# Optimization experiments

Measured on AMD Instinct MI355X. Metric: run time of the kernel, lower is better.

Reference implementation:

```python
import jax, jax.numpy as jnp
import numpy as np

N = 100000      # nodes
E = 3200000     # edges (avg degree 32)
IN = 256        # in_channels
OUT = 8         # out_channels
H1, C1 = 4, 4   # conv1: heads=4, out_channels=4 (concat -> 16)


def setup_inputs() -> dict:
    key = jax.random.key(0)
    ks = jax.random.split(key, 10)
    x = jax.random.normal(ks[0], (N, IN), jnp.float32)
    edge_index = jax.random.randint(ks[1], (2, E), 0, N, dtype=jnp.int64)

    def glorot(k, shape):
        fan_in = shape[0]
        return jax.random.normal(k, shape, jnp.float32) / np.float32(np.sqrt(fan_in))

    W1l = glorot(ks[2], (IN, H1 * C1))
    W1r = glorot(ks[3], (IN, H1 * C1))
    a1 = jax.random.normal(ks[4], (H1, C1), jnp.float32) / np.float32(np.sqrt(C1))
    b1 = jnp.zeros((H1 * C1,), jnp.float32)
    W2l = glorot(ks[5], (H1 * C1, OUT))
    W2r = glorot(ks[6], (H1 * C1, OUT))
    a2 = jax.random.normal(ks[7], (1, OUT), jnp.float32) / np.float32(np.sqrt(OUT))
    b2 = jnp.zeros((OUT,), jnp.float32)
    return {"x": x, "edge_index": edge_index, "W1l": W1l, "W1r": W1r, "a1": a1,
            "b1": b1, "W2l": W2l, "W2r": W2r, "a2": a2, "b2": b2}


def gatv2_conv(x, edge_index, Wl, Wr, att, bias, heads, ch, concat):
    # GATv2: e_ij = a^T LeakyReLU(Wl x_j + Wr x_i), softmax over incoming edges of i
    n = x.shape[0]
    src, dst = edge_index[0], edge_index[1]          # message flows src -> dst
    xl = (x @ Wl).reshape(n, heads, ch)              # [N,H,C] (source transform)
    xr = (x @ Wr).reshape(n, heads, ch)              # [N,H,C] (target transform)
    e = jax.nn.leaky_relu(xl[src] + xr[dst], 0.2)    # [E,H,C]
    logits = jnp.einsum('ehc,hc->eh', e, att)        # [E,H]
    # segment softmax over dst (stable: subtract per-target max)
    m = jax.ops.segment_max(logits, dst, num_segments=n)          # [N,H]
    ex = jnp.exp(logits - m[dst])                                  # [E,H]
    denom = jax.ops.segment_sum(ex, dst, num_segments=n)          # [N,H]
    alpha = ex / (denom[dst] + 1e-16)                              # [E,H]
    out = jax.ops.segment_sum(alpha[:, :, None] * xl[src], dst, num_segments=n)  # [N,H,C]
    out = out.reshape(n, heads * ch) if concat else out.mean(axis=1)
    return out + bias


def reference(x, edge_index, W1l, W1r, a1, b1, W2l, W2r, a2, b2):
    # eval mode: feature/attention dropout (p=0.6) are identity
    h = jax.nn.elu(gatv2_conv(x, edge_index, W1l, W1r, a1, b1, H1, C1, True))
    h = gatv2_conv(h, edge_index, W2l, W2r, a2, b2, 1, OUT, False)
    return jax.nn.sigmoid(h)
```

## Files before the change

### kernel.cpp

```cpp
#include <hip/hip_runtime.h>
#include <math.h>

#define NN 100000
#define NE 3200000
#define BW 512
#define BSH 9
#define NB 196
#define EPB_A 8192
#define NBLK_A ((NE + EPB_A - 1) / EPB_A)

__device__ __forceinline__ float lrelu(float v) { return v >= 0.f ? v : 0.2f * v; }


__global__ __launch_bounds__(256) void k_bhist(const int* __restrict__ dst,
                                               unsigned* __restrict__ btot) {
  __shared__ unsigned lh[NB];
  int tid = threadIdx.x;
  if (tid < NB) lh[tid] = 0;
  __syncthreads();
  int base = blockIdx.x * EPB_A;
  int end = min(base + EPB_A, NE);
  for (int e = base + tid * 4; e < end; e += 1024) {
    int4 d4 = *(const int4*)(dst + e);
    atomicAdd(&lh[((unsigned)d4.x) >> BSH], 1u);
    atomicAdd(&lh[((unsigned)d4.y) >> BSH], 1u);
    atomicAdd(&lh[((unsigned)d4.z) >> BSH], 1u);
    atomicAdd(&lh[((unsigned)d4.w) >> BSH], 1u);
  }
  __syncthreads();
  if (tid < NB && lh[tid]) atomicAdd(&btot[tid], lh[tid]);
}

__global__ __launch_bounds__(256) void k_bscan(const unsigned* __restrict__ btot,
    unsigned* __restrict__ bstart, unsigned* __restrict__ bcur) {
  __shared__ unsigned sm[256];
  int tid = threadIdx.x;
  unsigned v = (tid < NB) ? btot[tid] : 0;
  sm[tid] = v;
  __syncthreads();
  for (int off = 1; off < 256; off <<= 1) {
    unsigned u = (tid >= off) ? sm[tid - off] : 0;
    __syncthreads();
    sm[tid] += u;
    __syncthreads();
  }
  unsigned exc = sm[tid] - v;
  if (tid < NB) { bstart[tid] = exc; bcur[tid] = exc; }
  if (tid == NB - 1) bstart[NB] = sm[tid];
}

__global__ __launch_bounds__(256) void k_bin(const int* __restrict__ src,
    const int* __restrict__ dst, unsigned* __restrict__ bcur,
    unsigned* __restrict__ abuf) {
  __shared__ unsigned lh[NB], gb[NB], lcur[NB];
  int tid = threadIdx.x;
  if (tid < NB) lh[tid] = 0;
  __syncthreads();
  int base = blockIdx.x * EPB_A;
  int end = min(base + EPB_A, NE);
  for (int e = base + tid * 4; e < end; e += 1024) {
    int4 d4 = *(const int4*)(dst + e);
    atomicAdd(&lh[((unsigned)d4.x) >> BSH], 1u);
    atomicAdd(&lh[((unsigned)d4.y) >> BSH], 1u);
    atomicAdd(&lh[((unsigned)d4.z) >> BSH], 1u);
    atomicAdd(&lh[((unsigned)d4.w) >> BSH], 1u);
  }
  __syncthreads();
  if (tid < NB) {
    unsigned c = lh[tid];
    gb[tid] = c ? atomicAdd(&bcur[tid], c) : 0u;
    lcur[tid] = 0;
  }
  __syncthreads();
  for (int e = base + tid * 4; e < end; e += 1024) {
    int4 d4 = *(const int4*)(dst + e);
    int4 s4 = *(const int4*)(src + e);
    #pragma unroll
    for (int k = 0; k < 4; ++k) {
      unsigned d = (unsigned)(&d4.x)[k];
      unsigned s = (unsigned)(&s4.x)[k];
      unsigned b = d >> BSH;
      unsigned p = gb[b] + atomicAdd(&lcur[b], 1u);
      abuf[p] = ((d & (BW - 1)) << 17) | s;
    }
  }
}

__global__ __launch_bounds__(256) void k_bsort(const unsigned* __restrict__ bstart,
    const unsigned* __restrict__ abuf, int* __restrict__ rowstart,
    int* __restrict__ cnt, int* __restrict__ ssrc) {
  __shared__ unsigned lh[BW];
  __shared__ unsigned lcur[BW];
  __shared__ unsigned sm[256];
  int b = blockIdx.x, tid = threadIdx.x;
  unsigned s0 = bstart[b], s1 = bstart[b + 1];
  lh[tid] = 0; lh[tid + 256] = 0;
  __syncthreads();
  for (unsigned i = s0 + tid; i < s1; i += 256)
    atomicAdd(&lh[abuf[i] >> 17], 1u);
  __syncthreads();
  unsigned a0 = lh[2 * tid], a1 = lh[2 * tid + 1];
  sm[tid] = a0 + a1;
  __syncthreads();
  for (int off = 1; off < 256; off <<= 1) {
    unsigned u = (tid >= off) ? sm[tid - off] : 0;
    __syncthreads();
    sm[tid] += u;
    __syncthreads();
  }
  unsigned exc = sm[tid] - (a0 + a1);
  int node = b * BW + 2 * tid;
  if (node < NN)     { rowstart[node]     = s0 + exc;      cnt[node]     = a0; }
  if (node + 1 < NN) { rowstart[node + 1] = s0 + exc + a0; cnt[node + 1] = a1; }
  lcur[2 * tid] = exc;
  lcur[2 * tid + 1] = exc + a0;
  __syncthreads();
  for (unsigned i = s0 + tid; i < s1; i += 256) {
    unsigned v = abuf[i];
    unsigned p = s0 + atomicAdd(&lcur[v >> 17], 1u);
    ssrc[p] = (int)(v & 0x1FFFFu);
  }
}


__global__ __launch_bounds__(256) void k1_lin1(const float* __restrict__ x,
    const float* __restrict__ W1l, const float* __restrict__ W1r,
    float* __restrict__ xl1, float* __restrict__ xr1) {
  __shared__ float lw[256][32];
  int tid = threadIdx.x;
  for (int i = tid; i < 256 * 16; i += 256) {
    int k = i >> 4, c = i & 15;
    lw[k][c]      = W1l[i];
    lw[k][16 + c] = W1r[i];
  }
  __syncthreads();
  int row = blockIdx.x * 8 + (tid >> 5);
  if (row >= NN) return;
  int col = tid & 31;
  const float4* xrow = (const float4*)(x + (size_t)row * 256);
  float acc = 0.f;
  #pragma unroll 8
  for (int k4 = 0; k4 < 64; ++k4) {
    float4 xv = xrow[k4];
    int k = k4 << 2;
    acc = fmaf(xv.x, lw[k][col], acc);
    acc = fmaf(xv.y, lw[k + 1][col], acc);
    acc = fmaf(xv.z, lw[k + 2][col], acc);
    acc = fmaf(xv.w, lw[k + 3][col], acc);
  }
  if (col < 16) xl1[row * 16 + col] = acc;
  else          xr1[row * 16 + (col - 16)] = acc;
}


__global__ __launch_bounds__(256) void k_l1(const float* __restrict__ xl1,
    const float* __restrict__ xr1, const float* __restrict__ a1,
    const float* __restrict__ b1, const float* __restrict__ W2l,
    const float* __restrict__ W2r, const int* __restrict__ rowstart,
    const int* __restrict__ cnt, const int* __restrict__ ssrc,
    float* __restrict__ xl2, float* __restrict__ xr2) {
  __shared__ float w2[16][16];
  int tid = threadIdx.x;
  if (tid < 128) {
    int k = tid >> 3, c = tid & 7;
    w2[k][c]     = W2l[tid];
    w2[k][8 + c] = W2r[tid];
  }
  __syncthreads();
  int i = blockIdx.x * 256 + tid;
  if (i >= NN) return;

  float av[16];
  #pragma unroll
  for (int c = 0; c < 16; ++c) av[c] = a1[c];
  float xr[16];
  {
    const float4* xrp = (const float4*)(xr1 + (size_t)i * 16);
    #pragma unroll
    for (int q = 0; q < 4; ++q) *(float4*)&xr[q * 4] = xrp[q];
  }

  int rs = rowstart[i], deg = cnt[i];
  float m[4], den[4], acc[16];
  #pragma unroll
  for (int h = 0; h < 4; ++h) { m[h] = -INFINITY; den[h] = 0.f; }
  #pragma unroll
  for (int c = 0; c < 16; ++c) acc[c] = 0.f;

  float xn[16];
  if (deg > 0) {
    int s0 = ssrc[rs];
    const float4* xp = (const float4*)(xl1 + (size_t)s0 * 16);
    #pragma unroll
    for (int q = 0; q < 4; ++q) *(float4*)&xn[q * 4] = xp[q];
  }
  for (int j = 0; j < deg; ++j) {
    float xl[16];
    #pragma unroll
    for (int c = 0; c < 16; ++c) xl[c] = xn[c];
    if (j + 1 < deg) {
      int s = ssrc[rs + j + 1];
      const float4* xp = (const float4*)(xl1 + (size_t)s * 16);
      #pragma unroll
      for (int q = 0; q < 4; ++q) *(float4*)&xn[q * 4] = xp[q];
    }
    #pragma unroll
    for (int h = 0; h < 4; ++h) {
      float lg = lrelu(xl[h*4+0] + xr[h*4+0]) * av[h*4+0]
               + lrelu(xl[h*4+1] + xr[h*4+1]) * av[h*4+1]
               + lrelu(xl[h*4+2] + xr[h*4+2]) * av[h*4+2]
               + lrelu(xl[h*4+3] + xr[h*4+3]) * av[h*4+3];
      float nm = fmaxf(m[h], lg);
      float r = __expf(m[h] - nm);
      float p = __expf(lg - nm);
      m[h] = nm;
      den[h] = den[h] * r + p;
      #pragma unroll
      for (int c = 0; c < 4; ++c)
        acc[h*4+c] = acc[h*4+c] * r + p * xl[h*4+c];
    }
  }

  float hh[16];
  #pragma unroll
  for (int c = 0; c < 16; ++c) {
    float v = acc[c] / (den[c >> 2] + 1e-16f) + b1[c];
    hh[c] = v > 0.f ? v : expm1f(v);
  }
  float ol[8], orr[8];
  #pragma unroll
  for (int j = 0; j < 8; ++j) { ol[j] = 0.f; orr[j] = 0.f; }
  #pragma unroll
  for (int k = 0; k < 16; ++k) {
    float hv = hh[k];
    #pragma unroll
    for (int j = 0; j < 8; ++j) {
      ol[j]  = fmaf(hv, w2[k][j], ol[j]);
      orr[j] = fmaf(hv, w2[k][8 + j], orr[j]);
    }
  }
  *(float4*)(xl2 + (size_t)i * 8)     = make_float4(ol[0], ol[1], ol[2], ol[3]);
  *(float4*)(xl2 + (size_t)i * 8 + 4) = make_float4(ol[4], ol[5], ol[6], ol[7]);
  *(float4*)(xr2 + (size_t)i * 8)     = make_float4(orr[0], orr[1], orr[2], orr[3]);
  *(float4*)(xr2 + (size_t)i * 8 + 4) = make_float4(orr[4], orr[5], orr[6], orr[7]);
}


__global__ __launch_bounds__(256) void k_l2(const float* __restrict__ xl2,
    const float* __restrict__ xr2, const float* __restrict__ a2,
    const float* __restrict__ b2, const int* __restrict__ rowstart,
    const int* __restrict__ cnt, const int* __restrict__ ssrc,
    float* __restrict__ out) {
  int i = blockIdx.x * 256 + threadIdx.x;
  if (i >= NN) return;

  float av[8];
  #pragma unroll
  for (int c = 0; c < 8; ++c) av[c] = a2[c];
  float xr[8];
  {
    const float4* xrp = (const float4*)(xr2 + (size_t)i * 8);
    *(float4*)&xr[0] = xrp[0];
    *(float4*)&xr[4] = xrp[1];
  }

  int rs = rowstart[i], deg = cnt[i];
  float m = -INFINITY, den = 0.f, acc[8];
  #pragma unroll
  for (int c = 0; c < 8; ++c) acc[c] = 0.f;

  float xn[8];
  if (deg > 0) {
    int s0 = ssrc[rs];
    const float4* xp = (const float4*)(xl2 + (size_t)s0 * 8);
    *(float4*)&xn[0] = xp[0];
    *(float4*)&xn[4] = xp[1];
  }
  for (int j = 0; j < deg; ++j) {
    float xl[8];
    #pragma unroll
    for (int c = 0; c < 8; ++c) xl[c] = xn[c];
    if (j + 1 < deg) {
      int s = ssrc[rs + j + 1];
      const float4* xp = (const float4*)(xl2 + (size_t)s * 8);
      *(float4*)&xn[0] = xp[0];
      *(float4*)&xn[4] = xp[1];
    }
    float lg = 0.f;
    #pragma unroll
    for (int c = 0; c < 8; ++c) lg += lrelu(xl[c] + xr[c]) * av[c];
    float nm = fmaxf(m, lg);
    float r = __expf(m - nm);
    float p = __expf(lg - nm);
    m = nm;
    den = den * r + p;
    #pragma unroll
    for (int c = 0; c < 8; ++c) acc[c] = acc[c] * r + p * xl[c];
  }

  float o[8];
  #pragma unroll
  for (int c = 0; c < 8; ++c) {
    float v = acc[c] / (den + 1e-16f) + b2[c];
    o[c] = 1.f / (1.f + __expf(-v));
  }
  *(float4*)(out + (size_t)i * 8)     = make_float4(o[0], o[1], o[2], o[3]);
  *(float4*)(out + (size_t)i * 8 + 4) = make_float4(o[4], o[5], o[6], o[7]);
}


extern "C" void kernel_launch(void* const* d_in, const int* in_sizes, int n_in,
                              void* d_out, int out_size, void* d_ws, size_t ws_size,
                              hipStream_t stream) {
  const float* x   = (const float*)d_in[0];
  const int*   ei  = (const int*)d_in[1];
  const float* W1l = (const float*)d_in[2];
  const float* W1r = (const float*)d_in[3];
  const float* a1  = (const float*)d_in[4];
  const float* b1  = (const float*)d_in[5];
  const float* W2l = (const float*)d_in[6];
  const float* W2r = (const float*)d_in[7];
  const float* a2  = (const float*)d_in[8];
  const float* b2  = (const float*)d_in[9];
  const int* src = ei;
  const int* dst = ei + NE;

  char* ws = (char*)d_ws;
  size_t off = 0;
  auto alloc = [&](size_t bytes) { void* p = (void*)(ws + off); off += (bytes + 255) & ~(size_t)255; return p; };
  unsigned* btot   = (unsigned*)alloc((size_t)NB * 4);
  unsigned* bstart = (unsigned*)alloc((size_t)(NB + 1) * 4);
  unsigned* bcur   = (unsigned*)alloc((size_t)NB * 4);
  int*      rowstart = (int*)alloc((size_t)NN * 4);
  int*      cnt      = (int*)alloc((size_t)NN * 4);
  int*      ssrc     = (int*)alloc((size_t)NE * 4);
  char*     bigbase  = (char*)alloc((size_t)NN * 16 * 4 * 2);
  unsigned* abuf = (unsigned*)bigbase;
  float*    xl1  = (float*)bigbase;
  float*    xr1  = (float*)(bigbase + (size_t)NN * 16 * 4);
  float*    xl2  = (float*)alloc((size_t)NN * 8 * 4);
  float*    xr2  = (float*)alloc((size_t)NN * 8 * 4);

  hipMemsetAsync(btot, 0, (size_t)NB * 4, stream);

  k_bhist<<<NBLK_A, 256, 0, stream>>>(dst, btot);
  k_bscan<<<1, 256, 0, stream>>>(btot, bstart, bcur);
  k_bin  <<<NBLK_A, 256, 0, stream>>>(src, dst, bcur, abuf);
  k_bsort<<<NB, 256, 0, stream>>>(bstart, abuf, rowstart, cnt, ssrc);

  k1_lin1<<<(NN + 7) / 8, 256, 0, stream>>>(x, W1l, W1r, xl1, xr1);

  int gn = (NN + 255) / 256;
  k_l1<<<gn, 256, 0, stream>>>(xl1, xr1, a1, b1, W2l, W2r, rowstart, cnt, ssrc, xl2, xr2);
  k_l2<<<gn, 256, 0, stream>>>(xl2, xr2, a2, b2, rowstart, cnt, ssrc, (float*)d_out);
}
```

Baseline: 504.6 us.

## Use one wavefront per node for attention aggregation and thread-per-row linear

Both attention kernels now assign a 64-lane wavefront to each destination node. Neighbors are spread across lanes, and the kernel uses a chunked online softmax with shuffle max and sum reductions. Before, one thread walked the whole degree serially, with divergent, uncoalesced loads. The first linear layer switches from one thread per output column to one thread per row computing all 32 outputs, which reuses LDS weights via float4 broadcasts. The risks are wasted lanes for low-degree nodes (average degree 32 against wave width 64), more reduction overhead, and strided per-thread x row reads in lin1.

```diff
diff --git a/kernel.cpp b/kernel.cpp
--- a/kernel.cpp
+++ b/kernel.cpp
@@ -134,22 +134,45 @@
     lw[k][16 + c] = W1r[i];
   }
   __syncthreads();
-  int row = blockIdx.x * 8 + (tid >> 5);
+  int row = blockIdx.x * 256 + tid;
   if (row >= NN) return;
-  int col = tid & 31;
-  const float4* xrow = (const float4*)(x + (size_t)row * 256);
-  float acc = 0.f;
-  #pragma unroll 8
-  for (int k4 = 0; k4 < 64; ++k4) {
-    float4 xv = xrow[k4];
-    int k = k4 << 2;
-    acc = fmaf(xv.x, lw[k][col], acc);
-    acc = fmaf(xv.y, lw[k + 1][col], acc);
-    acc = fmaf(xv.z, lw[k + 2][col], acc);
-    acc = fmaf(xv.w, lw[k + 3][col], acc);
-  }
-  if (col < 16) xl1[row * 16 + col] = acc;
-  else          xr1[row * 16 + (col - 16)] = acc;
+  const float4* xr4 = (const float4*)(x + (size_t)row * 256);
+
+  float acc[32];
+  #pragma unroll
+  for (int c = 0; c < 32; ++c) acc[c] = 0.f;
+
+  float4 va = xr4[0], vb = xr4[1];
+  for (int k4 = 0; k4 < 64; k4 += 2) {
+    float4 vc = xr4[(k4 + 2) & 63];
+    float4 vd = xr4[(k4 + 3) & 63];
+    #pragma unroll
+    for (int half = 0; half < 2; ++half) {
+      float4 v = half ? vb : va;
+      int kb = (k4 + half) * 4;
+      #pragma unroll
+      for (int kk = 0; kk < 4; ++kk) {
+        float xk = (&v.x)[kk];
+        const float4* wrow = (const float4*)&lw[kb + kk][0];
+        #pragma unroll
+        for (int q = 0; q < 8; ++q) {
+          float4 w = wrow[q];
+          acc[q * 4 + 0] = fmaf(xk, w.x, acc[q * 4 + 0]);
+          acc[q * 4 + 1] = fmaf(xk, w.y, acc[q * 4 + 1]);
+          acc[q * 4 + 2] = fmaf(xk, w.z, acc[q * 4 + 2]);
+          acc[q * 4 + 3] = fmaf(xk, w.w, acc[q * 4 + 3]);
+        }
+      }
+    }
+    va = vc; vb = vd;
+  }
+  float4* ol = (float4*)(xl1 + (size_t)row * 16);
+  float4* orr = (float4*)(xr1 + (size_t)row * 16);
+  #pragma unroll
+  for (int q = 0; q < 4; ++q) {
+    ol[q]  = make_float4(acc[q*4+0], acc[q*4+1], acc[q*4+2], acc[q*4+3]);
+    orr[q] = make_float4(acc[16+q*4+0], acc[16+q*4+1], acc[16+q*4+2], acc[16+q*4+3]);
+  }
 }
 
 
@@ -167,82 +190,75 @@
     w2[k][8 + c] = W2r[tid];
   }
   __syncthreads();
-  int i = blockIdx.x * 256 + tid;
+  int i = (blockIdx.x * 256 + tid) >> 6;
   if (i >= NN) return;
-
-  float av[16];
-  #pragma unroll
-  for (int c = 0; c < 16; ++c) av[c] = a1[c];
-  float xr[16];
-  {
-    const float4* xrp = (const float4*)(xr1 + (size_t)i * 16);
-    #pragma unroll
-    for (int q = 0; q < 4; ++q) *(float4*)&xr[q * 4] = xrp[q];
-  }
-
+  int lane = tid & 63;
+  int j = lane >> 2, h = lane & 3;
+
+  float4 xr = *(const float4*)(xr1 + (size_t)i * 16 + h * 4);
+  float4 av = *(const float4*)(a1 + h * 4);
   int rs = rowstart[i], deg = cnt[i];
-  float m[4], den[4], acc[16];
-  #pragma unroll
-  for (int h = 0; h < 4; ++h) { m[h] = -INFINITY; den[h] = 0.f; }
-  #pragma unroll
-  for (int c = 0; c < 16; ++c) acc[c] = 0.f;
-
-  float xn[16];
-  if (deg > 0) {
-    int s0 = ssrc[rs];
-    const float4* xp = (const float4*)(xl1 + (size_t)s0 * 16);
-    #pragma unroll
-    for (int q = 0; q < 4; ++q) *(float4*)&xn[q * 4] = xp[q];
-  }
-  for (int j = 0; j < deg; ++j) {
-    float xl[16];
-    #pragma unroll
-    for (int c = 0; c < 16; ++c) xl[c] = xn[c];
-    if (j + 1 < deg) {
-      int s = ssrc[rs + j + 1];
-      const float4* xp = (const float4*)(xl1 + (size_t)s * 16);
-      #pragma unroll
-      for (int q = 0; q < 4; ++q) *(float4*)&xn[q * 4] = xp[q];
-    }
-    #pragma unroll
-    for (int h = 0; h < 4; ++h) {
-      float lg = lrelu(xl[h*4+0] + xr[h*4+0]) * av[h*4+0]
-               + lrelu(xl[h*4+1] + xr[h*4+1]) * av[h*4+1]
-               + lrelu(xl[h*4+2] + xr[h*4+2]) * av[h*4+2]
-               + lrelu(xl[h*4+3] + xr[h*4+3]) * av[h*4+3];
-      float nm = fmaxf(m[h], lg);
-      float r = __expf(m[h] - nm);
-      float p = __expf(lg - nm);
-      m[h] = nm;
-      den[h] = den[h] * r + p;
-      #pragma unroll
-      for (int c = 0; c < 4; ++c)
-        acc[h*4+c] = acc[h*4+c] * r + p * xl[h*4+c];
-    }
-  }
+
+  float m = -INFINITY, den = 0.f;
+  float4 acc = make_float4(0.f, 0.f, 0.f, 0.f);
+
+  for (int base = 0; base < deg; base += 16) {
+    int jj = base + j;
+    bool valid = jj < deg;
+    int s = valid ? ssrc[rs + jj] : 0;
+    float4 xl = make_float4(0.f, 0.f, 0.f, 0.f);
+    if (valid) xl = *(const float4*)(xl1 + (size_t)s * 16 + h * 4);
+    float lg = valid ? (lrelu(xl.x + xr.x) * av.x + lrelu(xl.y + xr.y) * av.y +
+                        lrelu(xl.z + xr.z) * av.z + lrelu(xl.w + xr.w) * av.w)
+                     : -INFINITY;
+    float mp = lg;
+    mp = fmaxf(mp, __shfl_xor(mp, 4));
+    mp = fmaxf(mp, __shfl_xor(mp, 8));
+    mp = fmaxf(mp, __shfl_xor(mp, 16));
+    mp = fmaxf(mp, __shfl_xor(mp, 32));
+    float nm = fmaxf(m, mp);
+    float r = __expf(m - nm);
+    float p = __expf(lg - nm);
+    m = nm;
+    den = den * r + p;
+    acc.x = acc.x * r + p * xl.x;
+    acc.y = acc.y * r + p * xl.y;
+    acc.z = acc.z * r + p * xl.z;
+    acc.w = acc.w * r + p * xl.w;
+  }
+  #pragma unroll
+  for (int st = 4; st <= 32; st <<= 1) {
+    den   += __shfl_xor(den, st);
+    acc.x += __shfl_xor(acc.x, st);
+    acc.y += __shfl_xor(acc.y, st);
+    acc.z += __shfl_xor(acc.z, st);
+    acc.w += __shfl_xor(acc.w, st);
+  }
+  float4 bv = *(const float4*)(b1 + h * 4);
+  float inv = 1.f / (den + 1e-16f);
+  float q0 = acc.x * inv + bv.x;
+  float q1 = acc.y * inv + bv.y;
+  float q2 = acc.z * inv + bv.z;
+  float q3 = acc.w * inv + bv.w;
+  q0 = q0 > 0.f ? q0 : expm1f(q0);
+  q1 = q1 > 0.f ? q1 : expm1f(q1);
+  q2 = q2 > 0.f ? q2 : expm1f(q2);
+  q3 = q3 > 0.f ? q3 : expm1f(q3);
 
   float hh[16];
   #pragma unroll
-  for (int c = 0; c < 16; ++c) {
-    float v = acc[c] / (den[c >> 2] + 1e-16f) + b1[c];
-    hh[c] = v > 0.f ? v : expm1f(v);
-  }
-  float ol[8], orr[8];
-  #pragma unroll
-  for (int j = 0; j < 8; ++j) { ol[j] = 0.f; orr[j] = 0.f; }
-  #pragma unroll
-  for (int k = 0; k < 16; ++k) {
-    float hv = hh[k];
-    #pragma unroll
-    for (int j = 0; j < 8; ++j) {
-      ol[j]  = fmaf(hv, w2[k][j], ol[j]);
-      orr[j] = fmaf(hv, w2[k][8 + j], orr[j]);
-    }
-  }
-  *(float4*)(xl2 + (size_t)i * 8)     = make_float4(ol[0], ol[1], ol[2], ol[3]);
-  *(float4*)(xl2 + (size_t)i * 8 + 4) = make_float4(ol[4], ol[5], ol[6], ol[7]);
-  *(float4*)(xr2 + (size_t)i * 8)     = make_float4(orr[0], orr[1], orr[2], orr[3]);
-  *(float4*)(xr2 + (size_t)i * 8 + 4) = make_float4(orr[4], orr[5], orr[6], orr[7]);
+  for (int hp = 0; hp < 4; ++hp) {
+    hh[hp * 4 + 0] = __shfl(q0, hp);
+    hh[hp * 4 + 1] = __shfl(q1, hp);
+    hh[hp * 4 + 2] = __shfl(q2, hp);
+    hh[hp * 4 + 3] = __shfl(q3, hp);
+  }
+  int t = lane & 15;
+  float val = 0.f;
+  #pragma unroll
+  for (int k = 0; k < 16; ++k) val = fmaf(hh[k], w2[k][t], val);
+  if (lane < 8)       xl2[(size_t)i * 8 + lane] = val;
+  else if (lane < 16) xr2[(size_t)i * 8 + (lane - 8)] = val;
 }
 
 
@@ -251,45 +267,43 @@
     const float* __restrict__ b2, const int* __restrict__ rowstart,
     const int* __restrict__ cnt, const int* __restrict__ ssrc,
     float* __restrict__ out) {
-  int i = blockIdx.x * 256 + threadIdx.x;
+  int tid = threadIdx.x;
+  int i = (blockIdx.x * 256 + tid) >> 6;
   if (i >= NN) return;
-
-  float av[8];
-  #pragma unroll
-  for (int c = 0; c < 8; ++c) av[c] = a2[c];
-  float xr[8];
-  {
-    const float4* xrp = (const float4*)(xr2 + (size_t)i * 8);
-    *(float4*)&xr[0] = xrp[0];
-    *(float4*)&xr[4] = xrp[1];
-  }
-
+  int lane = tid & 63;
+
+  float xr[8], av[8];
+  *(float4*)&xr[0] = *(const float4*)(xr2 + (size_t)i * 8);
+  *(float4*)&xr[4] = *(const float4*)(xr2 + (size_t)i * 8 + 4);
+  *(float4*)&av[0] = *(const float4*)(a2);
+  *(float4*)&av[4] = *(const float4*)(a2 + 4);
   int rs = rowstart[i], deg = cnt[i];
+
   float m = -INFINITY, den = 0.f, acc[8];
   #pragma unroll
   for (int c = 0; c < 8; ++c) acc[c] = 0.f;
 
-  float xn[8];
-  if (deg > 0) {
-    int s0 = ssrc[rs];
-    const float4* xp = (const float4*)(xl2 + (size_t)s0 * 8);
-    *(float4*)&xn[0] = xp[0];
-    *(float4*)&xn[4] = xp[1];
-  }
-  for (int j = 0; j < deg; ++j) {
+  for (int base = 0; base < deg; base += 64) {
+    int jj = base + lane;
+    bool valid = jj < deg;
+    int s = valid ? ssrc[rs + jj] : 0;
     float xl[8];
     #pragma unroll
-    for (int c = 0; c < 8; ++c) xl[c] = xn[c];
-    if (j + 1 < deg) {
-      int s = ssrc[rs + j + 1];
-      const float4* xp = (const float4*)(xl2 + (size_t)s * 8);
-      *(float4*)&xn[0] = xp[0];
-      *(float4*)&xn[4] = xp[1];
+    for (int c = 0; c < 8; ++c) xl[c] = 0.f;
+    if (valid) {
+      *(float4*)&xl[0] = *(const float4*)(xl2 + (size_t)s * 8);
+      *(float4*)&xl[4] = *(const float4*)(xl2 + (size_t)s * 8 + 4);
     }
-    float lg = 0.f;
-    #pragma unroll
-    for (int c = 0; c < 8; ++c) lg += lrelu(xl[c] + xr[c]) * av[c];
-    float nm = fmaxf(m, lg);
+    float lg;
+    if (valid) {
+      lg = 0.f;
+      #pragma unroll
+      for (int c = 0; c < 8; ++c) lg += lrelu(xl[c] + xr[c]) * av[c];
+    } else lg = -INFINITY;
+    float mp = lg;
+    #pragma unroll
+    for (int st = 1; st <= 32; st <<= 1) mp = fmaxf(mp, __shfl_xor(mp, st));
+    float nm = fmaxf(m, mp);
     float r = __expf(m - nm);
     float p = __expf(lg - nm);
     m = nm;
@@ -297,15 +311,23 @@
     #pragma unroll
     for (int c = 0; c < 8; ++c) acc[c] = acc[c] * r + p * xl[c];
   }
-
-  float o[8];
-  #pragma unroll
-  for (int c = 0; c < 8; ++c) {
-    float v = acc[c] / (den + 1e-16f) + b2[c];
-    o[c] = 1.f / (1.f + __expf(-v));
-  }
-  *(float4*)(out + (size_t)i * 8)     = make_float4(o[0], o[1], o[2], o[3]);
-  *(float4*)(out + (size_t)i * 8 + 4) = make_float4(o[4], o[5], o[6], o[7]);
+  #pragma unroll
+  for (int st = 1; st <= 32; st <<= 1) {
+    den += __shfl_xor(den, st);
+    #pragma unroll
+    for (int c = 0; c < 8; ++c) acc[c] += __shfl_xor(acc[c], st);
+  }
+  if (lane == 0) {
+    float inv = 1.f / (den + 1e-16f);
+    float o[8];
+    #pragma unroll
+    for (int c = 0; c < 8; ++c) {
+      float v = acc[c] * inv + b2[c];
+      o[c] = 1.f / (1.f + __expf(-v));
+    }
+    *(float4*)(out + (size_t)i * 8)     = make_float4(o[0], o[1], o[2], o[3]);
+    *(float4*)(out + (size_t)i * 8 + 4) = make_float4(o[4], o[5], o[6], o[7]);
+  }
 }
 
 
@@ -348,9 +370,9 @@
   k_bin  <<<NBLK_A, 256, 0, stream>>>(src, dst, bcur, abuf);
   k_bsort<<<NB, 256, 0, stream>>>(bstart, abuf, rowstart, cnt, ssrc);
 
-  k1_lin1<<<(NN + 7) / 8, 256, 0, stream>>>(x, W1l, W1r, xl1, xr1);
-
-  int gn = (NN + 255) / 256;
-  k_l1<<<gn, 256, 0, stream>>>(xl1, xr1, a1, b1, W2l, W2r, rowstart, cnt, ssrc, xl2, xr2);
-  k_l2<<<gn, 256, 0, stream>>>(xl2, xr2, a2, b2, rowstart, cnt, ssrc, (float*)d_out);
-}
+  k1_lin1<<<(NN + 255) / 256, 256, 0, stream>>>(x, W1l, W1r, xl1, xr1);
+
+  int gw = (NN * 64 + 255) / 256;
+  k_l1<<<gw, 256, 0, stream>>>(xl1, xr1, a1, b1, W2l, W2r, rowstart, cnt, ssrc, xl2, xr2);
+  k_l2<<<gw, 256, 0, stream>>>(xl2, xr2, a2, b2, rowstart, cnt, ssrc, (float*)d_out);
+}
```

Result: faster. 433.5 us (-14.1%).
